# Kernel tuning notes

Hardware: AMD Instinct MI355X
Metric: run time of the kernel (lower is better)

## Reference

```python
import jax, jax.numpy as jnp
import numpy as np
import math

N_HEAD = 12

def setup_inputs() -> dict:
    key = jax.random.key(0)
    ks = jax.random.split(key, 4)
    B, T, C = 4, 2048, 768
    x = jax.random.normal(ks[0], (B, T, C), dtype=jnp.float32)
    W_attn = jax.random.normal(ks[1], (C, 3 * C), dtype=jnp.float32) * (1.0 / math.sqrt(C))
    b_attn = jnp.zeros((3 * C,), dtype=jnp.float32)
    W_proj = jax.random.normal(ks[2], (C, C), dtype=jnp.float32) * (1.0 / math.sqrt(C))
    b_proj = jnp.zeros((C,), dtype=jnp.float32)
    decay_rates = jnp.full((N_HEAD,), 0.05, dtype=jnp.float32)
    return {"x": x, "W_attn": W_attn, "b_attn": b_attn,
            "W_proj": W_proj, "b_proj": b_proj, "decay_rates": decay_rates}

def reference(x, W_attn, b_attn, W_proj, b_proj, decay_rates):
    B, T, C = x.shape
    H = N_HEAD
    D = C // H
    qkv = x @ W_attn + b_attn                      # [B,T,3C]
    q, k, v = jnp.split(qkv, 3, axis=-1)
    q = q.reshape(B, T, H, D).transpose(0, 2, 1, 3)  # [B,H,T,D]
    k = k.reshape(B, T, H, D).transpose(0, 2, 1, 3)
    v = v.reshape(B, T, H, D).transpose(0, 2, 1, 3)
    att = jnp.einsum('bhqd,bhkd->bhqk', q, k) * (1.0 / math.sqrt(D))
    i = jnp.arange(T)[:, None]
    j = jnp.arange(T)[None, :]
    causal = i >= j                                  # [T,T]
    att = jnp.where(causal[None, None], att, -jnp.inf)
    att = jax.nn.softmax(att, axis=-1)
    # distances buffer: tril(j - i).abs() == (i - j) on the lower triangle, 0 above
    dist = jnp.where(causal, (i - j).astype(jnp.float32), 0.0)  # [T,T]
    decay = jnp.exp(-decay_rates[None, :, None, None] * dist[None, None])  # [1,H,T,T]
    att = att * decay
    att = att / (jnp.sum(att, axis=-1, keepdims=True) + 1e-8)
    y = jnp.einsum('bhqk,bhkd->bhqd', att, v)        # [B,H,T,D]
    y = y.transpose(0, 2, 1, 3).reshape(B, T, C)
    return y @ W_proj + b_proj
```

## Files before the change

### kernel.cpp

```cpp
#include <hip/hip_runtime.h>
#include <hip/hip_bf16.h>
#include <math.h>

#define T_ 2048
#define C_ 768
#define H_ 12
#define D_ 64
#define M_ 8192
#define QKV_N 2304

typedef short bf16x8 __attribute__((ext_vector_type(8)));
typedef float f32x4 __attribute__((ext_vector_type(4)));
typedef unsigned short u16;
typedef u16 u16x8 __attribute__((ext_vector_type(8)));
typedef u16 u16x4 __attribute__((ext_vector_type(4)));

__device__ u16 g_xb [M_*C_];
__device__ u16 g_wat[QKV_N*C_];
__device__ u16 g_wpt[C_*C_];
__device__ u16 g_q [M_*C_];
__device__ u16 g_k [M_*C_];
__device__ u16 g_vt[M_*C_];
__device__ u16 g_y [M_*C_];

__device__ __forceinline__ u16 f2bf(float f) {
    return __bfloat16_as_ushort(__float2bfloat16(f));
}
__device__ __forceinline__ f32x4 mfma16(bf16x8 a, bf16x8 b, f32x4 c) {
    return __builtin_amdgcn_mfma_f32_16x16x32_bf16(a, b, c, 0, 0, 0);
}
__device__ __forceinline__ void gl16(const u16* g, u16* l) {
    __builtin_amdgcn_global_load_lds(
        (const __attribute__((address_space(1))) unsigned int*)g,
        (__attribute__((address_space(3))) unsigned int*)l, 16, 0, 0);
}
__device__ __forceinline__ int ridx(int row, int chunk) {
    return row*64 + (((chunk) ^ (row & 7)) << 3);
}
__device__ __forceinline__ int swz(int row, int col) {
    return row*64 + ((((col >> 3) ^ (row & 7))) << 3) + (col & 7);
}

__global__ __launch_bounds__(256) void k_prep_x(const float* __restrict__ x)
{
    const int idx = blockIdx.x*256 + threadIdx.x;
    float4 a = ((const float4*)x)[idx*2];
    float4 b = ((const float4*)x)[idx*2+1];
    u16x8 o;
    o[0]=f2bf(a.x); o[1]=f2bf(a.y); o[2]=f2bf(a.z); o[3]=f2bf(a.w);
    o[4]=f2bf(b.x); o[5]=f2bf(b.y); o[6]=f2bf(b.z); o[7]=f2bf(b.w);
    ((u16x8*)g_xb)[idx] = o;
}

__global__ __launch_bounds__(256) void k_prep_w(const float* __restrict__ Wa,
                                                const float* __restrict__ Wp)
{
    __shared__ u16 L[64][72];
    const int tid = threadIdx.x;
    const int bx  = blockIdx.x;
    const int which = (bx >= QKV_N/64);
    const float* src = which ? Wp : Wa;
    const int N = which ? C_ : QKV_N;
    u16* dst = which ? g_wpt : g_wat;
    const int n0 = (which ? bx - QKV_N/64 : bx) * 64;
    const int k0 = blockIdx.y * 64;

    const int r  = tid >> 2;
    const int c0 = (tid & 3) * 16;
    const float* p = &src[(size_t)(k0 + r)*N + n0 + c0];
    float4 v[4];
    #pragma unroll
    for (int c = 0; c < 4; ++c) v[c] = ((const float4*)p)[c];
    const float* vf = (const float*)v;
    #pragma unroll
    for (int j = 0; j < 16; ++j) L[c0 + j][r] = f2bf(vf[j]);
    __syncthreads();
    const int nn = tid >> 2;
    const int s  = (tid & 3) * 16;
    *(u16x8*)&dst[(size_t)(n0+nn)*C_ + k0 + s]     = *(const u16x8*)&L[nn][s];
    *(u16x8*)&dst[(size_t)(n0+nn)*C_ + k0 + s + 8] = *(const u16x8*)&L[nn][s+8];
}

__global__ __launch_bounds__(256) void k_qkv(const float* __restrict__ bias)
{
    __shared__ u16 As[2][128*64];
    __shared__ u16 Bs[2][128*64];

    const int tid  = threadIdx.x;
    const int lane = tid & 63;
    const int wid  = tid >> 6;
    const int l15  = lane & 15;
    const int lg   = lane >> 4;
    const int wm = wid >> 1, wn = wid & 1;
    const int m0 = blockIdx.x * 128;
    const int n0 = blockIdx.y * 128;

    const int srow8 = lane >> 3;
    const int schk  = (lane & 7) ^ srow8;

    f32x4 acc[4][4];
    #pragma unroll
    for (int i = 0; i < 4; ++i)
        #pragma unroll
        for (int j = 0; j < 4; ++j) acc[i][j] = (f32x4){0.f,0.f,0.f,0.f};

    const u16* xa = &g_xb [(size_t)(m0 + wid*32 + srow8)*C_ + (schk<<3)];
    const u16* wb = &g_wat[(size_t)(n0 + wid*32 + srow8)*C_ + (schk<<3)];

    #pragma unroll
    for (int i = 0; i < 4; ++i) {
        const int r = wid*32 + i*8;
        gl16(xa + (size_t)i*8*C_,       &As[0][r*64]);
        gl16(wb + (size_t)i*8*C_,       &Bs[0][r*64]);
    }
    __syncthreads();

    int cur = 0;
    for (int k = 0; k < 12; ++k) {
        if (k < 11) {
            const int ko = (k+1)*64;
            #pragma unroll
            for (int i = 0; i < 4; ++i) {
                const int r = wid*32 + i*8;
                gl16(xa + (size_t)i*8*C_ + ko, &As[cur^1][r*64]);
                gl16(wb + (size_t)i*8*C_ + ko, &Bs[cur^1][r*64]);
            }
        }
        __builtin_amdgcn_s_setprio(1);
        #pragma unroll
        for (int kf = 0; kf < 2; ++kf) {
            bf16x8 bfr[4];
            #pragma unroll
            for (int nt = 0; nt < 4; ++nt) {
                const int rw = wn*64 + nt*16 + l15;
                bfr[nt] = *(const bf16x8*)&Bs[cur][ridx(rw, kf*4 + lg)];
            }
            #pragma unroll
            for (int mt = 0; mt < 4; ++mt) {
                const int rw = wm*64 + mt*16 + l15;
                bf16x8 afr = *(const bf16x8*)&As[cur][ridx(rw, kf*4 + lg)];
                #pragma unroll
                for (int nt = 0; nt < 4; ++nt)
                    acc[mt][nt] = mfma16(afr, bfr[nt], acc[mt][nt]);
            }
        }
        __builtin_amdgcn_s_setprio(0);
        __syncthreads();
        cur ^= 1;
    }

    const int nb    = n0 + wn*64;
    const int which = nb / C_;
    const int h     = (nb % C_) / D_;
    const int mbase = m0 + wm*64;
    const int bb    = mbase >> 11;
    const int bh    = bb*H_ + h;
    float bv4[4];
    #pragma unroll
    for (int nt = 0; nt < 4; ++nt) bv4[nt] = bias[nb + nt*16 + l15];

    if (which == 2) {
        #pragma unroll
        for (int mt = 0; mt < 4; ++mt) {
            const int tb = (mbase + mt*16 + lg*4) & (T_-1);
            #pragma unroll
            for (int nt = 0; nt < 4; ++nt) {
                const int d = nt*16 + l15;
                u16x4 pk;
                #pragma unroll
                for (int r = 0; r < 4; ++r) pk[r] = f2bf(acc[mt][nt][r] + bv4[nt]);
                *(u16x4*)&g_vt[((size_t)bh*D_ + d)*T_ + tb] = pk;
            }
        }
    } else {
        u16* dst = which ? g_k : g_q;
        #pragma unroll
        for (int mt = 0; mt < 4; ++mt)
            #pragma unroll
            for (int r = 0; r < 4; ++r) {
                const int t = (mbase + mt*16 + lg*4 + r) & (T_-1);
                #pragma unroll
                for (int nt = 0; nt < 4; ++nt)
                    dst[((size_t)bh*T_ + t)*D_ + nt*16 + l15] = f2bf(acc[mt][nt][r] + bv4[nt]);
            }
    }
}

__global__ __launch_bounds__(256) void k_attn(const float* __restrict__ rates)
{
    __shared__ u16 Ks[2][64*64];
    __shared__ u16 Vt[2][64*64];
    __shared__ u16 Ps[4][16*64];

    const int tid  = threadIdx.x;
    const int lane = tid & 63;
    const int wid  = tid >> 6;
    const int l15  = lane & 15;
    const int lg   = lane >> 4;

    const int id  = blockIdx.x;
    const int bh  = (id & 7)*6 + ((id >> 3) % 6);
    const int qt  = 31 - ((id >> 3) / 6);
    const int h   = bh % H_;
    const int bb  = bh / H_;
    const float rate = rates[h];
    const float LOG2E  = 1.4426950408889634f;
    const float srate  = rate * LOG2E;
    const float sscale = 0.125f * LOG2E;

    const int i0  = qt * 64;
    const int thr = wid*16 + l15;
    const int ig  = i0 + thr;

    const int wt = (int)(34.4f / (fmaxf(rate, 1e-8f) * 64.0f)) + 2;
    const int nT = min(qt + 1, wt);

    const u16* qb  = &g_q [(size_t)bh*T_*D_];
    const u16* kb  = &g_k [(size_t)bh*T_*D_];
    const u16* vtb = &g_vt[(size_t)bh*D_*T_];

    bf16x8 qf[2];
    qf[0] = *(const bf16x8*)&qb[(size_t)ig*D_ + lg*8];
    qf[1] = *(const bf16x8*)&qb[(size_t)ig*D_ + 32 + lg*8];

    float joff[16];
    #pragma unroll
    for (int t = 0; t < 4; ++t)
        #pragma unroll
        for (int r = 0; r < 4; ++r) joff[t*4+r] = srate * (float)(t*16 + lg*4 + r);

    f32x4 oAcc[4];
    #pragma unroll
    for (int n = 0; n < 4; ++n) oAcc[n] = (f32x4){0.f,0.f,0.f,0.f};
    float den = 0.f, mrow = 0.f;

    const int srow8 = lane >> 3;
    const int schk  = (lane & 7) ^ srow8;

    u16* PsW = &Ps[wid][0];

    #pragma unroll
    for (int i = 0; i < 2; ++i) {
        const int r = wid*16 + i*8;
        gl16(&kb [(size_t)(i0 + r + srow8)*D_ + (schk<<3)], &Ks[0][r*64]);
        gl16(&vtb[(size_t)(r + srow8)*T_ + i0 + (schk<<3)], &Vt[0][r*64]);
    }
    __syncthreads();

    int cur = 0;
    for (int tt = 0; tt < nT; ++tt) {
        const int j0 = i0 - tt*64;
        if (tt + 1 < nT) {
            const int jn = j0 - 64;
            #pragma unroll
            for (int i = 0; i < 2; ++i) {
                const int r = wid*16 + i*8;
                gl16(&kb [(size_t)(jn + r + srow8)*D_ + (schk<<3)], &Ks[cur^1][r*64]);
                gl16(&vtb[(size_t)(r + srow8)*T_ + jn + (schk<<3)], &Vt[cur^1][r*64]);
            }
        }

        __builtin_amdgcn_s_setprio(1);
        f32x4 sAcc[4];
        #pragma unroll
        for (int t = 0; t < 4; ++t) sAcc[t] = (f32x4){0.f,0.f,0.f,0.f};
        #pragma unroll
        for (int t = 0; t < 4; ++t)
            #pragma unroll
            for (int kf = 0; kf < 2; ++kf) {
                bf16x8 kfr = *(const bf16x8*)&Ks[cur][ridx(t*16 + l15, kf*4 + lg)];
                sAcc[t] = mfma16(kfr, qf[kf], sAcc[t]);
            }
        __builtin_amdgcn_s_setprio(0);

        float e[16];
        if (tt == 0) {
            const float sth = srate * (float)thr;
            float pv[16];
            float mx = -3e38f;
            #pragma unroll
            for (int t = 0; t < 4; ++t)
                #pragma unroll
                for (int r = 0; r < 4; ++r) {
                    const int jj = t*16 + lg*4 + r;
                    float v = fmaf(sAcc[t][r], sscale, joff[t*4+r] - sth);
                    if (jj > thr) v = -3e38f;
                    pv[t*4+r] = v;
                    mx = fmaxf(mx, v);
                }
            mx = fmaxf(mx, __shfl_xor(mx, 16, 64));
            mx = fmaxf(mx, __shfl_xor(mx, 32, 64));
            mrow = mx;
            #pragma unroll
            for (int i = 0; i < 16; ++i) {
                e[i] = __builtin_amdgcn_exp2f(pv[i] - mx);
                den += e[i];
            }
        } else {
            const float c0m = fmaf(srate, (float)(j0 - ig), -mrow);
            #pragma unroll
            for (int t = 0; t < 4; ++t)
                #pragma unroll
                for (int r = 0; r < 4; ++r) {
                    const float v = fmaf(sAcc[t][r], sscale, c0m + joff[t*4+r]);
                    const float p = __builtin_amdgcn_exp2f(v);
                    e[t*4+r] = p;
                    den += p;
                }
        }

        #pragma unroll
        for (int t = 0; t < 4; ++t) {
            u16x4 pk = { f2bf(e[t*4]), f2bf(e[t*4+1]), f2bf(e[t*4+2]), f2bf(e[t*4+3]) };
            *(u16x4*)&PsW[swz(l15, t*16 + lg*4)] = pk;
        }

        __builtin_amdgcn_s_setprio(1);
        #pragma unroll
        for (int kf = 0; kf < 2; ++kf) {
            bf16x8 pa = *(const bf16x8*)&PsW[ridx(l15, kf*4 + lg)];
            #pragma unroll
            for (int n = 0; n < 4; ++n) {
                bf16x8 vf = *(const bf16x8*)&Vt[cur][ridx(n*16 + l15, kf*4 + lg)];
                oAcc[n] = mfma16(pa, vf, oAcc[n]);
            }
        }
        __builtin_amdgcn_s_setprio(0);
        __syncthreads();
        cur ^= 1;
    }

    den += __shfl_xor(den, 16, 64);
    den += __shfl_xor(den, 32, 64);
    const float inv = 1.f / den;
    float ivr[4];
    #pragma unroll
    for (int r = 0; r < 4; ++r) ivr[r] = __shfl(inv, lg*4 + r, 64);
    #pragma unroll
    for (int r = 0; r < 4; ++r) {
        const int row = i0 + wid*16 + lg*4 + r;
        #pragma unroll
        for (int n = 0; n < 4; ++n)
            g_y[(size_t)(bb*T_ + row)*C_ + h*D_ + n*16 + l15] = f2bf(oAcc[n][r] * ivr[r]);
    }
}

__global__ __launch_bounds__(256) void k_proj(const float* __restrict__ bias,
                                              float* __restrict__ out)
{
    __shared__ u16 As[2][128*64];
    __shared__ u16 Bs[2][128*64];

    const int tid  = threadIdx.x;
    const int lane = tid & 63;
    const int wid  = tid >> 6;
    const int l15  = lane & 15;
    const int lg   = lane >> 4;
    const int wm = wid >> 1, wn = wid & 1;
    const int m0 = blockIdx.x * 128;
    const int n0 = blockIdx.y * 128;

    const int srow8 = lane >> 3;
    const int schk  = (lane & 7) ^ srow8;

    f32x4 acc[4][4];
    #pragma unroll
    for (int i = 0; i < 4; ++i)
        #pragma unroll
        for (int j = 0; j < 4; ++j) acc[i][j] = (f32x4){0.f,0.f,0.f,0.f};

    const u16* ya = &g_y  [(size_t)(m0 + wid*32 + srow8)*C_ + (schk<<3)];
    const u16* wb = &g_wpt[(size_t)(n0 + wid*32 + srow8)*C_ + (schk<<3)];

    #pragma unroll
    for (int i = 0; i < 4; ++i) {
        const int r = wid*32 + i*8;
        gl16(ya + (size_t)i*8*C_, &As[0][r*64]);
        gl16(wb + (size_t)i*8*C_, &Bs[0][r*64]);
    }
    __syncthreads();

    int cur = 0;
    for (int k = 0; k < 12; ++k) {
        if (k < 11) {
            const int ko = (k+1)*64;
            #pragma unroll
            for (int i = 0; i < 4; ++i) {
                const int r = wid*32 + i*8;
                gl16(ya + (size_t)i*8*C_ + ko, &As[cur^1][r*64]);
                gl16(wb + (size_t)i*8*C_ + ko, &Bs[cur^1][r*64]);
            }
        }
        __builtin_amdgcn_s_setprio(1);
        #pragma unroll
        for (int kf = 0; kf < 2; ++kf) {
            bf16x8 bfr[4];
            #pragma unroll
            for (int nt = 0; nt < 4; ++nt) {
                const int rw = wn*64 + nt*16 + l15;
                bfr[nt] = *(const bf16x8*)&Bs[cur][ridx(rw, kf*4 + lg)];
            }
            #pragma unroll
            for (int mt = 0; mt < 4; ++mt) {
                const int rw = wm*64 + mt*16 + l15;
                bf16x8 afr = *(const bf16x8*)&As[cur][ridx(rw, kf*4 + lg)];
                #pragma unroll
                for (int nt = 0; nt < 4; ++nt)
                    acc[mt][nt] = mfma16(afr, bfr[nt], acc[mt][nt]);
            }
        }
        __builtin_amdgcn_s_setprio(0);
        __syncthreads();
        cur ^= 1;
    }

    float bv4[4];
    #pragma unroll
    for (int nt = 0; nt < 4; ++nt) bv4[nt] = bias[n0 + wn*64 + nt*16 + l15];
    #pragma unroll
    for (int mt = 0; mt < 4; ++mt)
        #pragma unroll
        for (int r = 0; r < 4; ++r) {
            const int m = m0 + wm*64 + mt*16 + lg*4 + r;
            #pragma unroll
            for (int nt = 0; nt < 4; ++nt)
                out[(size_t)m*C_ + n0 + wn*64 + nt*16 + l15] = acc[mt][nt][r] + bv4[nt];
        }
}

extern "C" void kernel_launch(void* const* d_in, const int* in_sizes, int n_in,
                              void* d_out, int out_size, void* d_ws, size_t ws_size,
                              hipStream_t stream) {
    (void)in_sizes; (void)n_in; (void)d_ws; (void)ws_size; (void)out_size;
    const float* x      = (const float*)d_in[0];
    const float* W_attn = (const float*)d_in[1];
    const float* b_attn = (const float*)d_in[2];
    const float* W_proj = (const float*)d_in[3];
    const float* b_proj = (const float*)d_in[4];
    const float* rates  = (const float*)d_in[5];

    hipLaunchKernelGGL(k_prep_x, dim3(M_*C_/8/256), dim3(256), 0, stream, x);
    hipLaunchKernelGGL(k_prep_w, dim3(QKV_N/64 + C_/64, C_/64), dim3(256), 0, stream, W_attn, W_proj);
    hipLaunchKernelGGL(k_qkv,  dim3(M_/128, QKV_N/128), dim3(256), 0, stream, b_attn);
    hipLaunchKernelGGL(k_attn, dim3(1536),              dim3(256), 0, stream, rates);
    hipLaunchKernelGGL(k_proj, dim3(M_/128, C_/128),    dim3(256), 0, stream, b_proj, (float*)d_out);
}
```

Measured before the change: 196.1 us.

## Prefetch two stages ahead with explicit vmcnt waits in GEMM and attention loops

After: 197.2 us. About the same (+0.6%).

```diff
diff --git a/kernel.cpp b/kernel.cpp
--- a/kernel.cpp
+++ b/kernel.cpp
@@ -34,6 +34,10 @@
         (const __attribute__((address_space(1))) unsigned int*)g,
         (__attribute__((address_space(3))) unsigned int*)l, 16, 0, 0);
 }
+#define VMW(N)  asm volatile("s_waitcnt vmcnt(" #N ")" ::: "memory")
+#define SBAR()  __builtin_amdgcn_s_barrier()
+#define SFEN()  __builtin_amdgcn_sched_barrier(0)
+
 __device__ __forceinline__ int ridx(int row, int chunk) {
     return row*64 + (((chunk) ^ (row & 7)) << 3);
 }
@@ -81,6 +85,38 @@
     *(u16x8*)&dst[(size_t)(n0+nn)*C_ + k0 + s + 8] = *(const u16x8*)&L[nn][s+8];
 }
 
+__device__ __forceinline__ void stage2(const u16* a, const u16* b,
+                                       u16* As_, u16* Bs_, int ko, int wid)
+{
+    #pragma unroll
+    for (int i = 0; i < 4; ++i) {
+        const int r = wid*32 + i*8;
+        gl16(a + (size_t)i*8*C_ + ko, As_ + r*64);
+        gl16(b + (size_t)i*8*C_ + ko, Bs_ + r*64);
+    }
+}
+__device__ __forceinline__ void gemm_step(const u16* Asb, const u16* Bsb,
+                                          f32x4 (&acc)[4][4],
+                                          int wm, int wn, int l15, int lg)
+{
+    __builtin_amdgcn_s_setprio(1);
+    #pragma unroll
+    for (int kf = 0; kf < 2; ++kf) {
+        bf16x8 bfr[4];
+        #pragma unroll
+        for (int nt = 0; nt < 4; ++nt)
+            bfr[nt] = *(const bf16x8*)&Bsb[ridx(wn*64 + nt*16 + l15, kf*4 + lg)];
+        #pragma unroll
+        for (int mt = 0; mt < 4; ++mt) {
+            bf16x8 afr = *(const bf16x8*)&Asb[ridx(wm*64 + mt*16 + l15, kf*4 + lg)];
+            #pragma unroll
+            for (int nt = 0; nt < 4; ++nt)
+                acc[mt][nt] = mfma16(afr, bfr[nt], acc[mt][nt]);
+        }
+    }
+    __builtin_amdgcn_s_setprio(0);
+}
+
 __global__ __launch_bounds__(256) void k_qkv(const float* __restrict__ bias)
 {
     __shared__ u16 As[2][128*64];
@@ -107,45 +143,22 @@
     const u16* xa = &g_xb [(size_t)(m0 + wid*32 + srow8)*C_ + (schk<<3)];
     const u16* wb = &g_wat[(size_t)(n0 + wid*32 + srow8)*C_ + (schk<<3)];
 
-    #pragma unroll
-    for (int i = 0; i < 4; ++i) {
-        const int r = wid*32 + i*8;
-        gl16(xa + (size_t)i*8*C_,       &As[0][r*64]);
-        gl16(wb + (size_t)i*8*C_,       &Bs[0][r*64]);
-    }
-    __syncthreads();
+    stage2(xa, wb, As[0], Bs[0], 0,  wid);
+    stage2(xa, wb, As[1], Bs[1], 64, wid);
 
     int cur = 0;
+    #pragma unroll 1
     for (int k = 0; k < 12; ++k) {
-        if (k < 11) {
-            const int ko = (k+1)*64;
-            #pragma unroll
-            for (int i = 0; i < 4; ++i) {
-                const int r = wid*32 + i*8;
-                gl16(xa + (size_t)i*8*C_ + ko, &As[cur^1][r*64]);
-                gl16(wb + (size_t)i*8*C_ + ko, &Bs[cur^1][r*64]);
-            }
-        }
-        __builtin_amdgcn_s_setprio(1);
-        #pragma unroll
-        for (int kf = 0; kf < 2; ++kf) {
-            bf16x8 bfr[4];
-            #pragma unroll
-            for (int nt = 0; nt < 4; ++nt) {
-                const int rw = wn*64 + nt*16 + l15;
-                bfr[nt] = *(const bf16x8*)&Bs[cur][ridx(rw, kf*4 + lg)];
-            }
-            #pragma unroll
-            for (int mt = 0; mt < 4; ++mt) {
-                const int rw = wm*64 + mt*16 + l15;
-                bf16x8 afr = *(const bf16x8*)&As[cur][ridx(rw, kf*4 + lg)];
-                #pragma unroll
-                for (int nt = 0; nt < 4; ++nt)
-                    acc[mt][nt] = mfma16(afr, bfr[nt], acc[mt][nt]);
-            }
-        }
-        __builtin_amdgcn_s_setprio(0);
-        __syncthreads();
+        if (k < 11) { VMW(8); } else { VMW(0); }
+        SFEN();
+        SBAR();
+        SFEN();
+        gemm_step(As[cur], Bs[cur], acc, wm, wn, l15, lg);
+        if (k < 10) {
+            SBAR();
+            SFEN();
+            stage2(xa, wb, As[cur], Bs[cur], (k+2)*64, wid);
+        }
         cur ^= 1;
     }
 
@@ -239,26 +252,28 @@
 
     u16* PsW = &Ps[wid][0];
 
-    #pragma unroll
-    for (int i = 0; i < 2; ++i) {
-        const int r = wid*16 + i*8;
-        gl16(&kb [(size_t)(i0 + r + srow8)*D_ + (schk<<3)], &Ks[0][r*64]);
-        gl16(&vtb[(size_t)(r + srow8)*T_ + i0 + (schk<<3)], &Vt[0][r*64]);
-    }
-    __syncthreads();
+    #define ATTN_STAGE(J0, B) do {                                             \
+        _Pragma("unroll")                                                      \
+        for (int i_ = 0; i_ < 2; ++i_) {                                       \
+            const int r_ = wid*16 + i_*8;                                      \
+            gl16(&kb [(size_t)((J0) + r_ + srow8)*D_ + (schk<<3)], &Ks[B][r_*64]); \
+            gl16(&vtb[(size_t)(r_ + srow8)*T_ + (J0) + (schk<<3)], &Vt[B][r_*64]); \
+        } } while (0)
+
+    ATTN_STAGE(i0, 0);
+    if (nT > 1) ATTN_STAGE(i0 - 64, 1);
 
     int cur = 0;
+    #pragma unroll 1
     for (int tt = 0; tt < nT; ++tt) {
         const int j0 = i0 - tt*64;
-        if (tt + 1 < nT) {
-            const int jn = j0 - 64;
-            #pragma unroll
-            for (int i = 0; i < 2; ++i) {
-                const int r = wid*16 + i*8;
-                gl16(&kb [(size_t)(jn + r + srow8)*D_ + (schk<<3)], &Ks[cur^1][r*64]);
-                gl16(&vtb[(size_t)(r + srow8)*T_ + jn + (schk<<3)], &Vt[cur^1][r*64]);
-            }
-        }
+        if (tt + 1 < nT) { VMW(4); } else { VMW(0); }
+        SFEN();
+        SBAR();
+        SFEN();
+
+        const u16* Kc = Ks[cur];
+        const u16* Vc = Vt[cur];
 
         __builtin_amdgcn_s_setprio(1);
         f32x4 sAcc[4];
@@ -268,7 +283,7 @@
         for (int t = 0; t < 4; ++t)
             #pragma unroll
             for (int kf = 0; kf < 2; ++kf) {
-                bf16x8 kfr = *(const bf16x8*)&Ks[cur][ridx(t*16 + l15, kf*4 + lg)];
+                bf16x8 kfr = *(const bf16x8*)&Kc[ridx(t*16 + l15, kf*4 + lg)];
                 sAcc[t] = mfma16(kfr, qf[kf], sAcc[t]);
             }
         __builtin_amdgcn_s_setprio(0);
@@ -321,12 +336,17 @@
             bf16x8 pa = *(const bf16x8*)&PsW[ridx(l15, kf*4 + lg)];
             #pragma unroll
             for (int n = 0; n < 4; ++n) {
-                bf16x8 vf = *(const bf16x8*)&Vt[cur][ridx(n*16 + l15, kf*4 + lg)];
+                bf16x8 vf = *(const bf16x8*)&Vc[ridx(n*16 + l15, kf*4 + lg)];
                 oAcc[n] = mfma16(pa, vf, oAcc[n]);
             }
         }
         __builtin_amdgcn_s_setprio(0);
-        __syncthreads();
+
+        if (tt + 2 < nT) {
+            SBAR();
+            SFEN();
+            ATTN_STAGE(j0 - 128, cur);
+        }
         cur ^= 1;
     }
 
@@ -372,45 +392,22 @@
     const u16* ya = &g_y  [(size_t)(m0 + wid*32 + srow8)*C_ + (schk<<3)];
     const u16* wb = &g_wpt[(size_t)(n0 + wid*32 + srow8)*C_ + (schk<<3)];
 
-    #pragma unroll
-    for (int i = 0; i < 4; ++i) {
-        const int r = wid*32 + i*8;
-        gl16(ya + (size_t)i*8*C_, &As[0][r*64]);
-        gl16(wb + (size_t)i*8*C_, &Bs[0][r*64]);
-    }
-    __syncthreads();
+    stage2(ya, wb, As[0], Bs[0], 0,  wid);
+    stage2(ya, wb, As[1], Bs[1], 64, wid);
 
     int cur = 0;
+    #pragma unroll 1
     for (int k = 0; k < 12; ++k) {
-        if (k < 11) {
-            const int ko = (k+1)*64;
-            #pragma unroll
-            for (int i = 0; i < 4; ++i) {
-                const int r = wid*32 + i*8;
-                gl16(ya + (size_t)i*8*C_ + ko, &As[cur^1][r*64]);
-                gl16(wb + (size_t)i*8*C_ + ko, &Bs[cur^1][r*64]);
-            }
-        }
-        __builtin_amdgcn_s_setprio(1);
-        #pragma unroll
-        for (int kf = 0; kf < 2; ++kf) {
-            bf16x8 bfr[4];
-            #pragma unroll
-            for (int nt = 0; nt < 4; ++nt) {
-                const int rw = wn*64 + nt*16 + l15;
-                bfr[nt] = *(const bf16x8*)&Bs[cur][ridx(rw, kf*4 + lg)];
-            }
-            #pragma unroll
-            for (int mt = 0; mt < 4; ++mt) {
-                const int rw = wm*64 + mt*16 + l15;
-                bf16x8 afr = *(const bf16x8*)&As[cur][ridx(rw, kf*4 + lg)];
-                #pragma unroll
-                for (int nt = 0; nt < 4; ++nt)
-                    acc[mt][nt] = mfma16(afr, bfr[nt], acc[mt][nt]);
-            }
-        }
-        __builtin_amdgcn_s_setprio(0);
-        __syncthreads();
+        if (k < 11) { VMW(8); } else { VMW(0); }
+        SFEN();
+        SBAR();
+        SFEN();
+        gemm_step(As[cur], Bs[cur], acc, wm, wn, l15, lg);
+        if (k < 10) {
+            SBAR();
+            SFEN();
+            stage2(ya, wb, As[cur], Bs[cur], (k+2)*64, wid);
+        }
         cur ^= 1;
     }
 
```
